# Performance work log

Measured on AMD Instinct MI355X. Metric: run time of the kernel, lower is better.

The kernel has to match this reference:

```python
import jax, jax.numpy as jnp
import numpy as np

B, S, D = 2, 2048, 2048
H, HD = 16, 128
ROPE_THETA = 10000.0


def _rope_cos_sin(seq_len, head_dim, dtype=jnp.float32):
    inv_freq = 1.0 / (ROPE_THETA ** (jnp.arange(0, head_dim, 2, dtype=jnp.float32) / head_dim))
    t = jnp.arange(seq_len, dtype=jnp.float32)
    freqs = jnp.outer(t, inv_freq)                     # [S, HD/2]
    emb = jnp.concatenate([freqs, freqs], axis=-1)     # [S, HD]
    return jnp.cos(emb).astype(dtype), jnp.sin(emb).astype(dtype)


def _rotate_half(x):
    x1, x2 = jnp.split(x, 2, axis=-1)
    return jnp.concatenate([-x2, x1], axis=-1)


def _apply_rope(x, cos, sin):
    # x: [B, S, H, HD]; cos/sin: [S, HD] -> broadcast over batch and heads
    c = cos[None, :, None, :]
    s = sin[None, :, None, :]
    return x * c + _rotate_half(x) * s


def setup_inputs() -> dict:
    key = jax.random.key(0)
    ks = jax.random.split(key, 6)
    scale = 1.0 / np.sqrt(D)
    hidden_states = jax.random.normal(ks[0], (B, S, D), dtype=jnp.float32)
    # causal additive mask: 0 on/below diagonal, large negative above
    neg = jnp.finfo(jnp.float32).min
    causal = jnp.where(jnp.tril(jnp.ones((S, S), dtype=bool)), 0.0, neg)
    attention_mask = jnp.broadcast_to(causal[None, None, :, :], (B, 1, S, S)).astype(jnp.float32)
    Wq = jax.random.normal(ks[1], (D, D), dtype=jnp.float32) * scale
    Wk = jax.random.normal(ks[2], (D, D), dtype=jnp.float32) * scale
    Wv = jax.random.normal(ks[3], (D, D), dtype=jnp.float32) * scale
    Wo = jax.random.normal(ks[4], (D, D), dtype=jnp.float32) * scale
    return {"hidden_states": hidden_states, "attention_mask": attention_mask,
            "Wq": Wq, "Wk": Wk, "Wv": Wv, "Wo": Wo}


def reference(hidden_states, attention_mask, Wq, Wk, Wv, Wo):
    b, s, d = hidden_states.shape
    # projections (torch Linear: x @ W^T)
    q = (hidden_states @ Wq.T).reshape(b, s, H, HD)
    k = (hidden_states @ Wk.T).reshape(b, s, H, HD)
    v = (hidden_states @ Wv.T).reshape(b, s, H, HD)
    cos, sin = _rope_cos_sin(s, HD, hidden_states.dtype)
    q = _apply_rope(q, cos, sin)
    k = _apply_rope(k, cos, sin)
    # naive attention, [B, H, S, S] scores materialized as in the original
    scores = jnp.einsum('bqhd,bkhd->bhqk', q, k) / np.sqrt(HD)
    scores = scores + attention_mask
    attn = jax.nn.softmax(scores, axis=-1)
    out = jnp.einsum('bhqk,bkhd->bqhd', attn, v).reshape(b, s, d)
    return out @ Wo.T
```

## Files before the change

kernel.cpp:

```cpp
#include <hip/hip_runtime.h>
#include <hip/hip_bf16.h>

typedef __hip_bfloat16 bf16;
typedef __attribute__((ext_vector_type(8))) short s16x8;
typedef __attribute__((ext_vector_type(4))) float f32x4;
typedef __attribute__((ext_vector_type(16))) float f32x16;

#define MFMA16(a, b, c) __builtin_amdgcn_mfma_f32_16x16x32_bf16(a, b, c, 0, 0, 0)
#define MFMA32(a, b, c) __builtin_amdgcn_mfma_f32_32x32x16_bf16(a, b, c, 0, 0, 0)

#define GLL16(gsrc, ldst)                                                                 \
  __builtin_amdgcn_global_load_lds(                                                       \
      (const __attribute__((address_space(1))) unsigned int*)(gsrc),                      \
      (__attribute__((address_space(3))) unsigned int*)(ldst), 16, 0, 0)

#define VMCNT(n) asm volatile("s_waitcnt vmcnt(" #n ")" ::: "memory")
#define BARRIER() __builtin_amdgcn_s_barrier()

static constexpr int S_LEN = 2048;
static constexpr int D_DIM = 2048;
static constexpr int NY = 6144;

union BF4 { ushort4 u; bf16 b[4]; };

__device__ inline unsigned pack2(float a, float b) {
  union { bf16 h[2]; unsigned u; } x;
  x.h[0] = __float2bfloat16(a);
  x.h[1] = __float2bfloat16(b);
  return x.u;
}

__global__ void convert_all(const float* __restrict__ X, const float* __restrict__ Wq,
                            const float* __restrict__ Wk, const float* __restrict__ Wv,
                            const float* __restrict__ Wo, bf16* __restrict__ Xb,
                            bf16* __restrict__ Wb, bf16* __restrict__ Wob,
                            float* __restrict__ cosT, float* __restrict__ sinT) {
  int gid = blockIdx.x * 256 + threadIdx.x;
  if (gid < 6291456) {
    int i4 = gid * 4;
    const float* src;
    bf16* dst;
    int off;
    if (i4 < 8388608) {
      src = X; dst = Xb; off = i4;
    } else {
      int j = i4 - 8388608;
      int seg = j >> 22;
      off = j & 4194303;
      if (seg == 0) { src = Wq; dst = Wb; }
      else if (seg == 1) { src = Wk; dst = Wb + 4194304; }
      else if (seg == 2) { src = Wv; dst = Wb + 8388608; }
      else { src = Wo; dst = Wob; }
    }
    float4 v = *(const float4*)(src + off);
    BF4 o;
    o.b[0] = __float2bfloat16(v.x);
    o.b[1] = __float2bfloat16(v.y);
    o.b[2] = __float2bfloat16(v.z);
    o.b[3] = __float2bfloat16(v.w);
    *(ushort4*)(dst + off) = o.u;
  } else {
    int t4 = (gid - 6291456) * 4;
    if (t4 < 131072) {
#pragma unroll
      for (int k = 0; k < 4; ++k) {
        int i = t4 + k;
        int d = i & 63, s = i >> 6;
        float inv = powf(10000.0f, -(float)d * (1.0f / 64.0f));
        float ang = (float)s * inv;
        cosT[i] = cosf(ang);
        sinT[i] = sinf(ang);
      }
    }
  }
}

__global__ __launch_bounds__(256) void rope_tv(bf16* __restrict__ Y,
                                               const float* __restrict__ cosT,
                                               const float* __restrict__ sinT,
                                               bf16* __restrict__ Vt) {
  __shared__ bf16 tile[32][36];
  const int bid = blockIdx.x;
  const int t = threadIdx.x;
  if (bid < 8192) {
    int idx = bid * 256 + t;
    int quad = idx & 15;
    int h = (idx >> 4) & 15;
    int m = (idx >> 8) & 4095;
    int g = idx >> 20;
    int s = m & (S_LEN - 1);
    int d0 = quad * 4;
    float sc = g ? 1.0f : 0.08838834764831845f * 1.4426950408889634f;
    bf16* p = Y + (size_t)m * NY + g * D_DIM + h * 128 + d0;
    BF4 lo, hi, olo, ohi;
    lo.u = *(const ushort4*)p;
    hi.u = *(const ushort4*)(p + 64);
    float4 c = *(const float4*)(cosT + s * 64 + d0);
    float4 sn = *(const float4*)(sinT + s * 64 + d0);
    float cc[4] = {c.x, c.y, c.z, c.w};
    float ss[4] = {sn.x, sn.y, sn.z, sn.w};
#pragma unroll
    for (int i = 0; i < 4; ++i) {
      float x1 = __bfloat162float(lo.b[i]);
      float x2 = __bfloat162float(hi.b[i]);
      olo.b[i] = __float2bfloat16((x1 * cc[i] - x2 * ss[i]) * sc);
      ohi.b[i] = __float2bfloat16((x2 * cc[i] + x1 * ss[i]) * sc);
    }
    *(ushort4*)p = olo.u;
    *(ushort4*)(p + 64) = ohi.u;
  } else {
    int id = bid - 8192;
    int bx = id & 63, by = (id >> 6) & 3, bh = id >> 8;
    int b = bh >> 4, h = bh & 15;
    int s0 = bx * 32, d0 = by * 32;
    int r = t >> 3;
    int c4 = (t & 7) * 4;
    BF4 in;
    in.u = *(const ushort4*)(Y + (size_t)(b * S_LEN + s0 + r) * NY + 4096 + h * 128 + d0 + c4);
    *(ushort4*)(&tile[r][c4]) = in.u;
    __syncthreads();
    BF4 o;
#pragma unroll
    for (int i = 0; i < 4; ++i) o.b[i] = tile[c4 + i][r];
    *(ushort4*)(Vt + (size_t)bh * 128 * S_LEN + (size_t)(d0 + r) * S_LEN + s0 + c4) = o.u;
  }
}

__device__ inline void storeC(float* p, float v) { *p = v; }
__device__ inline void storeC(bf16* p, float v) { *p = __float2bfloat16(v); }

__global__ __launch_bounds__(512, 2) void gemm256(const bf16* __restrict__ A,
                                                  const bf16* __restrict__ Bm,
                                                  bf16* __restrict__ C, int K, int lda,
                                                  int ldb, int ldc, int mt) {
  __shared__ __align__(16) char lds[131072];
  char* A0buf = lds;
  char* B0buf = lds + 32768;
  char* A1buf = lds + 65536;
  char* B1buf = lds + 98304;
  const int tid = threadIdx.x;
  const int lane = tid & 63;
  const int w = tid >> 6;
  const int wm = w >> 2, wn = w & 3;
  const int l15 = lane & 15, lh4 = lane >> 4;
  const int xr = l15 & 7;
  const int xo0 = ((lh4 ^ xr) << 4);
  const int xo1 = (((4 + lh4) ^ xr) << 4);

  const int nwg = gridDim.x;
  const int bid = blockIdx.x;
  const int swz = (bid & 7) * (nwg >> 3) + (bid >> 3);
  const int bm = swz % mt, bn = swz / mt;
  const int row0 = bm * 256, col0 = bn * 256;

  const int srow8 = lane >> 3;
  const int scol = ((lane & 7) ^ srow8) * 8;
  const bf16* gA_s = A + (size_t)(row0 + w * 8 + srow8) * lda + scol;
  const bf16* gB_s = Bm + (size_t)(col0 + (w >> 2) * 64 + (w & 3) * 8 + srow8) * ldb + scol;
  const int ldst = w * 1024;

#define STAGE_A(bufa, rh, k0)                                                     \
  {                                                                               \
    GLL16(gA_s + (size_t)((rh)*64) * lda + (k0), (bufa) + (rh)*16384 + ldst);     \
    GLL16(gA_s + (size_t)((rh)*64 + 128) * lda + (k0),                            \
          (bufa) + (rh)*16384 + 8192 + ldst);                                     \
  }
#define STAGE_B(bufb, ch, k0)                                                     \
  {                                                                               \
    GLL16(gB_s + (size_t)((ch)*32) * ldb + (k0), (bufb) + (ch)*16384 + ldst);     \
    GLL16(gB_s + (size_t)((ch)*32 + 128) * ldb + (k0),                            \
          (bufb) + (ch)*16384 + 8192 + ldst);                                     \
  }

  f32x4 acc[8][4];
#pragma unroll
  for (int i = 0; i < 8; ++i)
#pragma unroll
    for (int j = 0; j < 4; ++j) acc[i][j] = (f32x4){0.f, 0.f, 0.f, 0.f};

  s16x8 af[4][2];
  s16x8 bfr[2][2];

#define READ_AH(bufa, rh)                                                         \
  _Pragma("unroll") for (int ii = 0; ii < 4; ++ii) {                              \
    const char* p_ = (bufa) + (rh)*16384 + (wm * 64 + ii * 16 + l15) * 128;       \
    af[ii][0] = *(const s16x8*)(p_ + xo0);                                        \
    af[ii][1] = *(const s16x8*)(p_ + xo1);                                        \
  }
#define READ_BH(bufb, ch)                                                         \
  _Pragma("unroll") for (int jj = 0; jj < 2; ++jj) {                              \
    const char* p_ = (bufb) + (ch)*16384 + (wn * 32 + jj * 16 + l15) * 128;       \
    bfr[jj][0] = *(const s16x8*)(p_ + xo0);                                       \
    bfr[jj][1] = *(const s16x8*)(p_ + xo1);                                       \
  }
#define QUAD(rh, ch)                                                              \
  __builtin_amdgcn_s_setprio(1);                                                  \
  _Pragma("unroll") for (int jj = 0; jj < 2; ++jj)                                \
  _Pragma("unroll") for (int ii = 0; ii < 4; ++ii)                                \
  _Pragma("unroll") for (int ks = 0; ks < 2; ++ks)                                \
      acc[(rh)*4 + ii][(ch)*2 + jj] =                                             \
          MFMA16(af[ii][ks], bfr[jj][ks], acc[(rh)*4 + ii][(ch)*2 + jj]);         \
  __builtin_amdgcn_s_setprio(0);

  STAGE_A(A0buf, 0, 0);
  STAGE_B(B0buf, 0, 0);
  STAGE_B(B0buf, 1, 0);
  STAGE_A(A0buf, 1, 0);
  STAGE_A(A1buf, 0, 64);
  STAGE_B(B1buf, 1, 64);
  STAGE_A(A1buf, 1, 64);
  VMCNT(6);
  BARRIER();

  const int NI = K >> 7;
  for (int i = 0; i < NI; ++i) {
    const int kT1 = (2 * i + 1) << 6;
    const int kT2 = (2 * i + 2) << 6;
    const int kT3 = (2 * i + 3) << 6;
    const bool nl = (i + 1 < NI);
    READ_AH(A0buf, 0);
    READ_BH(B0buf, 0);
    STAGE_B(B1buf, 0, kT1);
    BARRIER();
    QUAD(0, 0);
    BARRIER();
    READ_BH(B0buf, 1);
    if (nl) STAGE_A(A0buf, 0, kT2);
    BARRIER();
    QUAD(0, 1);
    BARRIER();
    READ_AH(A0buf, 1);
    if (nl) STAGE_B(B0buf, 1, kT2);
    BARRIER();
    QUAD(1, 1);
    BARRIER();
    READ_BH(B0buf, 0);
    if (nl) STAGE_A(A0buf, 1, kT2);
    BARRIER();
    QUAD(1, 0);
    if (nl) { VMCNT(6); } else { VMCNT(0); }
    BARRIER();
    READ_AH(A1buf, 0);
    READ_BH(B1buf, 0);
    if (nl) STAGE_B(B0buf, 0, kT2);
    BARRIER();
    QUAD(0, 0);
    BARRIER();
    READ_BH(B1buf, 1);
    if (nl) STAGE_A(A1buf, 0, kT3);
    BARRIER();
    QUAD(0, 1);
    BARRIER();
    READ_AH(A1buf, 1);
    if (nl) STAGE_B(B1buf, 1, kT3);
    BARRIER();
    QUAD(1, 1);
    BARRIER();
    READ_BH(B1buf, 0);
    if (nl) STAGE_A(A1buf, 1, kT3);
    BARRIER();
    QUAD(1, 0);
    if (nl) { VMCNT(6); }
    BARRIER();
  }
#undef STAGE_A
#undef STAGE_B
#undef READ_AH
#undef READ_BH
#undef QUAD

#pragma unroll
  for (int ri = 0; ri < 8; ++ri)
#pragma unroll
    for (int cj = 0; cj < 4; ++cj) {
      int gr = row0 + wm * 128 + ri * 16 + lh4 * 4;
      int gc = col0 + wn * 64 + cj * 16 + l15;
#pragma unroll
      for (int rr = 0; rr < 4; ++rr)
        C[(size_t)(gr + rr) * ldc + gc] = __float2bfloat16(acc[ri][cj][rr]);
    }
}

template <typename OutT>
__global__ __launch_bounds__(512, 2) void gemm_fine(const bf16* __restrict__ A,
                                                    const bf16* __restrict__ Bm,
                                                    OutT* __restrict__ C, int K, int lda,
                                                    int ldb, int ldc, int mt) {
  __shared__ __align__(16) char lds[147456];
  char* b0 = lds;
  char* b1 = lds + 49152;
  char* b2 = lds + 98304;
  const int tid = threadIdx.x;
  const int lane = tid & 63;
  const int w = tid >> 6;
  const int wm = w >> 2, wn = w & 3;
  const int l15 = lane & 15, lh4 = lane >> 4;
  const int xr = l15 & 7;
  const int xo0 = ((lh4 ^ xr) << 4);
  const int xo1 = (((4 + lh4) ^ xr) << 4);

  const int nwg = gridDim.x;
  const int bid = blockIdx.x;
  const int swz = (bid & 7) * (nwg >> 3) + (bid >> 3);
  const int bm = swz % mt, bn = swz / mt;
  const int row0 = bm * 128, col0 = bn * 256;

  const int srow = w * 8 + (lane >> 3);
  const int scol = ((lane & 7) ^ (lane >> 3)) * 8;
  const bf16* gA = A + (size_t)(row0 + srow) * lda + scol;
  const bf16* gB = Bm + (size_t)(col0 + srow) * ldb + scol;
  const int ldst = w * 1024;

  f32x4 acc[4][4];
#pragma unroll
  for (int i = 0; i < 4; ++i)
#pragma unroll
    for (int j = 0; j < 4; ++j) acc[i][j] = (f32x4){0.f, 0.f, 0.f, 0.f};

  s16x8 af[4], bfr[4];

#define PH_READ(BUF, XO)                                                          \
  _Pragma("unroll") for (int ii = 0; ii < 4; ++ii)                                \
      af[ii] = *(const s16x8*)((BUF) + (wm * 64 + ii * 16 + l15) * 128 + (XO));   \
  _Pragma("unroll") for (int jj = 0; jj < 4; ++jj)                                \
      bfr[jj] = *(const s16x8*)((BUF) + 16384 + (wn * 64 + jj * 16 + l15) * 128 + (XO));
#define PH_FMA()                                                                  \
  __builtin_amdgcn_s_setprio(1);                                                  \
  _Pragma("unroll") for (int jj = 0; jj < 4; ++jj)                                \
  _Pragma("unroll") for (int ii = 0; ii < 4; ++ii)                                \
      acc[ii][jj] = MFMA16(af[ii], bfr[jj], acc[ii][jj]);                         \
  __builtin_amdgcn_s_setprio(0);
#define STAGE_T(BUF, kS)                                                          \
  GLL16(gA + (kS), (BUF) + ldst);                                                 \
  GLL16(gA + (size_t)64 * lda + (kS), (BUF) + 8192 + ldst);                       \
  GLL16(gB + (kS), (BUF) + 16384 + ldst);                                         \
  GLL16(gB + (size_t)64 * ldb + (kS), (BUF) + 24576 + ldst);                      \
  GLL16(gB + (size_t)128 * ldb + (kS), (BUF) + 32768 + ldst);                     \
  GLL16(gB + (size_t)192 * ldb + (kS), (BUF) + 40960 + ldst);
#define TILE_MAIN(RBUF, SBUF, kS)                                                 \
  PH_READ(RBUF, xo0);                                                             \
  GLL16(gA + (kS), (SBUF) + ldst);                                                \
  GLL16(gA + (size_t)64 * lda + (kS), (SBUF) + 8192 + ldst);                      \
  GLL16(gB + (kS), (SBUF) + 16384 + ldst);                                        \
  BARRIER();                                                                      \
  PH_FMA();                                                                       \
  BARRIER();                                                                      \
  PH_READ(RBUF, xo1);                                                             \
  GLL16(gB + (size_t)64 * ldb + (kS), (SBUF) + 24576 + ldst);                     \
  GLL16(gB + (size_t)128 * ldb + (kS), (SBUF) + 32768 + ldst);                    \
  GLL16(gB + (size_t)192 * ldb + (kS), (SBUF) + 40960 + ldst);                    \
  BARRIER();                                                                      \
  PH_FMA();                                                                       \
  VMCNT(6);                                                                       \
  BARRIER();

  STAGE_T(b0, 0);
  STAGE_T(b1, 64);
  VMCNT(6);
  BARRIER();

  const int NT = K >> 6;
  for (int t = 0; t < NT - 2; t += 3) {
    TILE_MAIN(b0, b2, (size_t)(t + 2) * 64);
    TILE_MAIN(b1, b0, (size_t)(t + 3) * 64);
    TILE_MAIN(b2, b1, (size_t)(t + 4) * 64);
  }
  PH_READ(b0, xo0);
  BARRIER();
  PH_FMA();
  BARRIER();
  PH_READ(b0, xo1);
  BARRIER();
  PH_FMA();
  VMCNT(0);
  BARRIER();
  PH_READ(b1, xo0);
  BARRIER();
  PH_FMA();
  BARRIER();
  PH_READ(b1, xo1);
  BARRIER();
  PH_FMA();
#undef PH_READ
#undef PH_FMA
#undef STAGE_T
#undef TILE_MAIN

#pragma unroll
  for (int mi = 0; mi < 4; ++mi)
#pragma unroll
    for (int ni = 0; ni < 4; ++ni) {
      int gr = row0 + wm * 64 + mi * 16 + lh4 * 4;
      int gc = col0 + wn * 64 + ni * 16 + l15;
#pragma unroll
      for (int rr = 0; rr < 4; ++rr)
        storeC(&C[(size_t)(gr + rr) * ldc + gc], acc[mi][ni][rr]);
    }
}

__global__ __launch_bounds__(256, 2) void attn_fwd(const bf16* __restrict__ Y,
                                                   const bf16* __restrict__ Vt,
                                                   bf16* __restrict__ At) {
  __shared__ __align__(16) char smem[65536];

  const int idx = blockIdx.x;
  const int qt = 15 - (idx >> 5);
  const int bh = idx & 31;
  const int b = bh >> 4, h = bh & 15;
  const int tid = threadIdx.x;
  const int lane = tid & 63;
  const int w = tid >> 6;
  const int l31 = lane & 31;
  const int hi = lane >> 5;
  const int q0w = qt * 128 + w * 32;
  const int q = q0w + l31;

  s16x8 qf[8];
  {
    const bf16* qb = Y + (size_t)(b * S_LEN + q) * NY + h * 128 + hi * 8;
#pragma unroll
    for (int s = 0; s < 8; ++s) qf[s] = *(const s16x8*)(qb + s * 16);
  }

  f32x16 O[4];
#pragma unroll
  for (int d = 0; d < 4; ++d)
#pragma unroll
    for (int e = 0; e < 16; ++e) O[d][e] = 0.f;
  float m_run = -3.0e38f, l_run = 0.f;

  const bf16* Kbase = Y + (size_t)(b * S_LEN) * NY + 2048 + h * 128;
  const bf16* Vbase = Vt + (size_t)bh * 128 * S_LEN;
  const int tmax = 2 * qt + 1;

  const int rk_ = w * 4 + (lane >> 4);
  const int ck_ = lane & 15;
  const int dv_ = w * 8 + (lane >> 3);
  const int cv_ = lane & 7;

#define STAGE_KV(T, BASE)                                                         \
  {                                                                               \
    const int kv0s = (T)*64;                                                      \
    _Pragma("unroll") for (int j = 0; j < 4; ++j) {                               \
      int rk = j * 16 + rk_;                                                      \
      GLL16(Kbase + (size_t)(kv0s + rk) * NY + ((ck_ ^ (rk & 15)) * 8),           \
            (BASE) + (j * 4096 + w * 1024));                                      \
      int dv = j * 32 + dv_;                                                      \
      GLL16(Vbase + (size_t)dv * S_LEN + kv0s + ((cv_ ^ (dv & 7)) * 8),           \
            (BASE) + 16384 + (j * 4096 + w * 1024));                              \
    }                                                                             \
  }

  STAGE_KV(0, smem);

  for (int t = 0; t <= tmax; ++t) {
    const int kv0 = t * 64;
    const char* cur = smem + (t & 1) * 32768;
    BARRIER();
    if (t < tmax) {
      STAGE_KV(t + 1, smem + ((t + 1) & 1) * 32768);
      VMCNT(8);
    } else {
      VMCNT(0);
    }
    BARRIER();
    if (kv0 > q0w + 31) continue;

    float sv[32];
#pragma unroll
    for (int tt = 0; tt < 2; ++tt) {
      f32x16 sa;
#pragma unroll
      for (int e = 0; e < 16; ++e) sa[e] = 0.f;
      const int rk = tt * 32 + l31;
      const char* kr = cur + rk * 256;
      const int xr = (rk & 15) << 4;
#pragma unroll
      for (int s = 0; s < 8; ++s) {
        s16x8 kf = *(const s16x8*)(kr + ((s * 32 + hi * 16) ^ xr));
        sa = MFMA32(kf, qf[s], sa);
      }
#pragma unroll
      for (int e = 0; e < 16; ++e) sv[tt * 16 + e] = sa[e];
    }

    if (kv0 + 63 > q0w) {
#pragma unroll
      for (int tt = 0; tt < 2; ++tt)
#pragma unroll
        for (int r = 0; r < 16; ++r) {
          int kvr = kv0 + tt * 32 + (r & 3) + 8 * (r >> 2) + 4 * hi;
          if (kvr > q) sv[tt * 16 + r] = -3.0e38f;
        }
    }

    float mx[16];
#pragma unroll
    for (int i = 0; i < 16; ++i) mx[i] = fmaxf(sv[i], sv[i + 16]);
#pragma unroll
    for (int st = 8; st >= 1; st >>= 1)
#pragma unroll
      for (int i = 0; i < 8; ++i)
        if (i < st) mx[i] = fmaxf(mx[i], mx[i + st]);
    float pmax = fmaxf(mx[0], __shfl_xor(mx[0], 32, 64));

    bool need = pmax > m_run + 11.54f;
    if (__any(need)) {
      float newm = fmaxf(m_run, pmax);
      float ef = exp2f(m_run - newm);
      m_run = newm;
      l_run *= ef;
#pragma unroll
      for (int d = 0; d < 4; ++d)
#pragma unroll
        for (int e = 0; e < 16; ++e) O[d][e] *= ef;
    }

    float rsum = 0.f;
#pragma unroll
    for (int i = 0; i < 32; ++i) {
      sv[i] = exp2f(sv[i] - m_run);
      rsum += sv[i];
    }
    rsum += __shfl_xor(rsum, 32, 64);
    l_run += rsum;

    unsigned pw[4][4];
#pragma unroll
    for (int tt = 0; tt < 2; ++tt) {
      const int bs = tt * 16;
      unsigned x01 = pack2(sv[bs + 0], sv[bs + 1]);
      unsigned x23 = pack2(sv[bs + 2], sv[bs + 3]);
      unsigned x45 = pack2(sv[bs + 4], sv[bs + 5]);
      unsigned x67 = pack2(sv[bs + 6], sv[bs + 7]);
      unsigned y01 = pack2(sv[bs + 8], sv[bs + 9]);
      unsigned y23 = pack2(sv[bs + 10], sv[bs + 11]);
      unsigned y45 = pack2(sv[bs + 12], sv[bs + 13]);
      unsigned y67 = pack2(sv[bs + 14], sv[bs + 15]);
      asm volatile("v_permlane32_swap_b32 %0, %1" : "+v"(x01), "+v"(x45));
      asm volatile("v_permlane32_swap_b32 %0, %1" : "+v"(x23), "+v"(x67));
      asm volatile("v_permlane32_swap_b32 %0, %1" : "+v"(y01), "+v"(y45));
      asm volatile("v_permlane32_swap_b32 %0, %1" : "+v"(y23), "+v"(y67));
      pw[tt * 2][0] = x01;
      pw[tt * 2][1] = x23;
      pw[tt * 2][2] = x45;
      pw[tt * 2][3] = x67;
      pw[tt * 2 + 1][0] = y01;
      pw[tt * 2 + 1][1] = y23;
      pw[tt * 2 + 1][2] = y45;
      pw[tt * 2 + 1][3] = y67;
    }

#pragma unroll
    for (int dt = 0; dt < 4; ++dt) {
      const int d = dt * 32 + l31;
      const char* vr = cur + 16384 + d * 128;
      const int xv = (d & 7) << 4;
#pragma unroll
      for (int sl = 0; sl < 4; ++sl) {
        s16x8 vf = *(const s16x8*)(vr + ((sl * 32 + hi * 16) ^ xv));
        union { unsigned u[4]; s16x8 v; } pb;
        pb.u[0] = pw[sl][0];
        pb.u[1] = pw[sl][1];
        pb.u[2] = pw[sl][2];
        pb.u[3] = pw[sl][3];
        O[dt] = MFMA32(vf, pb.v, O[dt]);
      }
    }
  }
#undef STAGE_KV

  __syncthreads();
  const float inv = 1.0f / l_run;
  {
    const int orow = w * 32 + l31;
    const int xo = (orow & 15) << 4;
    char* obase = (char*)smem + orow * 256;
#pragma unroll
    for (int dt = 0; dt < 4; ++dt)
#pragma unroll
      for (int r = 0; r < 16; ++r) {
        int d = dt * 32 + (r & 3) + 8 * (r >> 2) + 4 * hi;
        *(bf16*)(obase + ((d * 2) ^ xo)) = __float2bfloat16(O[dt][r] * inv);
      }
  }
  __syncthreads();
  bf16* dst = At + (size_t)(b * S_LEN + qt * 128) * D_DIM + h * 128;
#pragma unroll
  for (int j = 0; j < 8; ++j) {
    int id = j * 256 + tid;
    int rr = id >> 4, cc = id & 15;
    int4 val = *(const int4*)((char*)smem + rr * 256 + ((cc * 16) ^ ((rr & 15) << 4)));
    *(int4*)(dst + (size_t)rr * D_DIM + cc * 8) = val;
  }
}

extern "C" void kernel_launch(void* const* d_in, const int* in_sizes, int n_in,
                              void* d_out, int out_size, void* d_ws, size_t ws_size,
                              hipStream_t stream) {
  const float* X = (const float*)d_in[0];
  const float* Wq = (const float*)d_in[2];
  const float* Wk = (const float*)d_in[3];
  const float* Wv = (const float*)d_in[4];
  const float* Wo = (const float*)d_in[5];
  float* out = (float*)d_out;
  char* ws = (char*)d_ws;

  bf16* Xb = (bf16*)(ws);
  bf16* Wb = (bf16*)(ws + 16777216);
  bf16* Wob = (bf16*)(ws + 41943040);
  bf16* Y = (bf16*)(ws + 50331648);
  bf16* Vt = (bf16*)(ws + 100663296);
  bf16* At = (bf16*)(ws + 117440512);
  float* cosT = (float*)(ws + 134217728);
  float* sinT = (float*)(ws + 134742016);

  convert_all<<<24704, 256, 0, stream>>>(X, Wq, Wk, Wv, Wo, Xb, Wb, Wob, cosT, sinT);

  gemm256<<<256, 512, 0, stream>>>(Xb, Wb, Y, 2048, 2048, 2048, 6144, 16);
  gemm_fine<bf16><<<256, 512, 0, stream>>>(Xb, Wb + (size_t)4096 * 2048, Y + 4096,
                                           2048, 2048, 2048, 6144, 32);
  rope_tv<<<16384, 256, 0, stream>>>(Y, cosT, sinT, Vt);
  attn_fwd<<<512, 256, 0, stream>>>(Y, Vt, At);
  gemm_fine<float><<<256, 512, 0, stream>>>(At, Wob, out, 2048, 2048, 2048, 2048, 32);
}
```

Baseline: 247.8 us.

## Software-pipeline attention: overlap next QK^T with current softmax and PV

Restructures the causal flash-attention loop so the QK^T MFMA for tile t+1 is issued before the softmax and PV of tile t, with K double-buffered and V triple-buffered in a larger LDS allocation. It also adds s_setprio around MFMA blocks, splits QK accumulation into two independent chains, and uses tree reductions for max and sum. The launch index mapping now handles blocks beyond 256. The goal is to hide MFMA and exp latency behind each other, at the cost of more registers and LDS (80KB), which may lower occupancy relative to the requested 2 blocks per CU.

```diff
diff --git a/kernel.cpp b/kernel.cpp
--- a/kernel.cpp
+++ b/kernel.cpp
@@ -401,10 +401,10 @@
 __global__ __launch_bounds__(256, 2) void attn_fwd(const bf16* __restrict__ Y,
                                                    const bf16* __restrict__ Vt,
                                                    bf16* __restrict__ At) {
-  __shared__ __align__(16) char smem[65536];
+  __shared__ __align__(16) char smem[81920];
 
   const int idx = blockIdx.x;
-  const int qt = 15 - (idx >> 5);
+  const int qt = (idx < 256) ? (15 - (idx >> 5)) : ((idx - 256) >> 5);
   const int bh = idx & 31;
   const int b = bh >> 4, h = bh & 15;
   const int tid = threadIdx.x;
@@ -412,6 +412,7 @@
   const int w = tid >> 6;
   const int l31 = lane & 31;
   const int hi = lane >> 5;
+  const int hi4 = hi * 4;
   const int q0w = qt * 128 + w * 32;
   const int q = q0w + l31;
 
@@ -437,138 +438,166 @@
   const int ck_ = lane & 15;
   const int dv_ = w * 8 + (lane >> 3);
   const int cv_ = lane & 7;
-
-#define STAGE_KV(T, BASE)                                                         \
+  char* const Vlds = smem + 32768;
+
+#define STAGE_KV(T, KOFF, VOFF)                                                   \
   {                                                                               \
     const int kv0s = (T)*64;                                                      \
     _Pragma("unroll") for (int j = 0; j < 4; ++j) {                               \
       int rk = j * 16 + rk_;                                                      \
       GLL16(Kbase + (size_t)(kv0s + rk) * NY + ((ck_ ^ (rk & 15)) * 8),           \
-            (BASE) + (j * 4096 + w * 1024));                                      \
+            smem + (KOFF) + (j * 4096 + w * 1024));                               \
       int dv = j * 32 + dv_;                                                      \
       GLL16(Vbase + (size_t)dv * S_LEN + kv0s + ((cv_ ^ (dv & 7)) * 8),           \
-            (BASE) + 16384 + (j * 4096 + w * 1024));                              \
+            Vlds + (VOFF) + (j * 4096 + w * 1024));                               \
     }                                                                             \
   }
 
-  STAGE_KV(0, smem);
-
-  for (int t = 0; t <= tmax; ++t) {
-    const int kv0 = t * 64;
-    const char* cur = smem + (t & 1) * 32768;
-    BARRIER();
-    if (t < tmax) {
-      STAGE_KV(t + 1, smem + ((t + 1) & 1) * 32768);
-      VMCNT(8);
-    } else {
-      VMCNT(0);
-    }
-    BARRIER();
-    if (kv0 > q0w + 31) continue;
-
-    float sv[32];
-#pragma unroll
-    for (int tt = 0; tt < 2; ++tt) {
-      f32x16 sa;
-#pragma unroll
-      for (int e = 0; e < 16; ++e) sa[e] = 0.f;
-      const int rk = tt * 32 + l31;
-      const char* kr = cur + rk * 256;
-      const int xr = (rk & 15) << 4;
-#pragma unroll
-      for (int s = 0; s < 8; ++s) {
-        s16x8 kf = *(const s16x8*)(kr + ((s * 32 + hi * 16) ^ xr));
-        sa = MFMA32(kf, qf[s], sa);
-      }
-#pragma unroll
-      for (int e = 0; e < 16; ++e) sv[tt * 16 + e] = sa[e];
-    }
-
-    if (kv0 + 63 > q0w) {
-#pragma unroll
-      for (int tt = 0; tt < 2; ++tt)
-#pragma unroll
-        for (int r = 0; r < 16; ++r) {
-          int kvr = kv0 + tt * 32 + (r & 3) + 8 * (r >> 2) + 4 * hi;
-          if (kvr > q) sv[tt * 16 + r] = -3.0e38f;
-        }
-    }
-
-    float mx[16];
-#pragma unroll
-    for (int i = 0; i < 16; ++i) mx[i] = fmaxf(sv[i], sv[i + 16]);
-#pragma unroll
-    for (int st = 8; st >= 1; st >>= 1)
-#pragma unroll
-      for (int i = 0; i < 8; ++i)
-        if (i < st) mx[i] = fmaxf(mx[i], mx[i + st]);
-    float pmax = fmaxf(mx[0], __shfl_xor(mx[0], 32, 64));
-
-    bool need = pmax > m_run + 11.54f;
-    if (__any(need)) {
-      float newm = fmaxf(m_run, pmax);
-      float ef = exp2f(m_run - newm);
-      m_run = newm;
-      l_run *= ef;
-#pragma unroll
-      for (int d = 0; d < 4; ++d)
-#pragma unroll
-        for (int e = 0; e < 16; ++e) O[d][e] *= ef;
-    }
-
-    float rsum = 0.f;
-#pragma unroll
-    for (int i = 0; i < 32; ++i) {
-      sv[i] = exp2f(sv[i] - m_run);
-      rsum += sv[i];
-    }
-    rsum += __shfl_xor(rsum, 32, 64);
-    l_run += rsum;
-
-    unsigned pw[4][4];
-#pragma unroll
-    for (int tt = 0; tt < 2; ++tt) {
-      const int bs = tt * 16;
-      unsigned x01 = pack2(sv[bs + 0], sv[bs + 1]);
-      unsigned x23 = pack2(sv[bs + 2], sv[bs + 3]);
-      unsigned x45 = pack2(sv[bs + 4], sv[bs + 5]);
-      unsigned x67 = pack2(sv[bs + 6], sv[bs + 7]);
-      unsigned y01 = pack2(sv[bs + 8], sv[bs + 9]);
-      unsigned y23 = pack2(sv[bs + 10], sv[bs + 11]);
-      unsigned y45 = pack2(sv[bs + 12], sv[bs + 13]);
-      unsigned y67 = pack2(sv[bs + 14], sv[bs + 15]);
-      asm volatile("v_permlane32_swap_b32 %0, %1" : "+v"(x01), "+v"(x45));
-      asm volatile("v_permlane32_swap_b32 %0, %1" : "+v"(x23), "+v"(x67));
-      asm volatile("v_permlane32_swap_b32 %0, %1" : "+v"(y01), "+v"(y45));
-      asm volatile("v_permlane32_swap_b32 %0, %1" : "+v"(y23), "+v"(y67));
-      pw[tt * 2][0] = x01;
-      pw[tt * 2][1] = x23;
-      pw[tt * 2][2] = x45;
-      pw[tt * 2][3] = x67;
-      pw[tt * 2 + 1][0] = y01;
-      pw[tt * 2 + 1][1] = y23;
-      pw[tt * 2 + 1][2] = y45;
-      pw[tt * 2 + 1][3] = y67;
-    }
-
-#pragma unroll
-    for (int dt = 0; dt < 4; ++dt) {
-      const int d = dt * 32 + l31;
-      const char* vr = cur + 16384 + d * 128;
-      const int xv = (d & 7) << 4;
-#pragma unroll
-      for (int sl = 0; sl < 4; ++sl) {
-        s16x8 vf = *(const s16x8*)(vr + ((sl * 32 + hi * 16) ^ xv));
-        union { unsigned u[4]; s16x8 v; } pb;
-        pb.u[0] = pw[sl][0];
-        pb.u[1] = pw[sl][1];
-        pb.u[2] = pw[sl][2];
-        pb.u[3] = pw[sl][3];
-        O[dt] = MFMA32(vf, pb.v, O[dt]);
-      }
-    }
-  }
+#define QKT(SVC, KOFF)                                                            \
+  {                                                                               \
+    __builtin_amdgcn_s_setprio(1);                                                \
+    _Pragma("unroll") for (int tt = 0; tt < 2; ++tt) {                            \
+      f32x16 se, so;                                                              \
+      _Pragma("unroll") for (int e = 0; e < 16; ++e) { se[e] = 0.f; so[e] = 0.f; }\
+      const int rk = tt * 32 + l31;                                               \
+      const char* kr = smem + (KOFF) + rk * 256;                                  \
+      const int xrr = (rk & 15) << 4;                                             \
+      _Pragma("unroll") for (int s = 0; s < 8; s += 2) {                          \
+        s16x8 kf0 = *(const s16x8*)(kr + ((s * 32 + hi * 16) ^ xrr));             \
+        se = MFMA32(kf0, qf[s], se);                                              \
+        s16x8 kf1 = *(const s16x8*)(kr + (((s + 1) * 32 + hi * 16) ^ xrr));       \
+        so = MFMA32(kf1, qf[s + 1], so);                                          \
+      }                                                                           \
+      _Pragma("unroll") for (int e = 0; e < 16; ++e) SVC[tt * 16 + e] = se[e] + so[e]; \
+    }                                                                             \
+    __builtin_amdgcn_s_setprio(0);                                                \
+  }
+
+#define FIN_A(SVP, KV0P)                                                          \
+  {                                                                               \
+    if ((KV0P) + 63 > q0w) {                                                      \
+      const int thr = q - (KV0P);                                                 \
+      _Pragma("unroll") for (int tt = 0; tt < 2; ++tt)                            \
+      _Pragma("unroll") for (int r = 0; r < 16; ++r) {                            \
+        const int c = tt * 32 + (r & 3) + 8 * (r >> 2);                           \
+        SVP[tt * 16 + r] = (c + hi4 > thr) ? -3.0e38f : SVP[tt * 16 + r];         \
+      }                                                                           \
+    }                                                                             \
+    float m8[8];                                                                  \
+    _Pragma("unroll") for (int i = 0; i < 8; ++i)                                 \
+        m8[i] = fmaxf(fmaxf(SVP[i], SVP[i + 8]), fmaxf(SVP[i + 16], SVP[i + 24]));\
+    float m2a = fmaxf(fmaxf(m8[0], m8[1]), fmaxf(m8[2], m8[3]));                  \
+    float m2b = fmaxf(fmaxf(m8[4], m8[5]), fmaxf(m8[6], m8[7]));                  \
+    float mloc = fmaxf(m2a, m2b);                                                 \
+    float pmax = fmaxf(mloc, __shfl_xor(mloc, 32, 64));                           \
+    bool need = pmax > m_run + 11.54f;                                            \
+    if (__any(need)) {                                                            \
+      float newm = fmaxf(m_run, pmax);                                            \
+      float ef = exp2f(m_run - newm);                                             \
+      m_run = newm;                                                               \
+      l_run *= ef;                                                                \
+      _Pragma("unroll") for (int d = 0; d < 4; ++d)                               \
+      _Pragma("unroll") for (int e = 0; e < 16; ++e) O[d][e] *= ef;               \
+    }                                                                             \
+  }
+
+#define FIN_B(SVP, VOFF)                                                          \
+  {                                                                               \
+    _Pragma("unroll") for (int i = 0; i < 32; ++i) SVP[i] = exp2f(SVP[i] - m_run);\
+    float s16v[16];                                                               \
+    _Pragma("unroll") for (int i = 0; i < 16; ++i) s16v[i] = SVP[i] + SVP[i + 16];\
+    float s8v[8];                                                                 \
+    _Pragma("unroll") for (int i = 0; i < 8; ++i) s8v[i] = s16v[i] + s16v[i + 8]; \
+    float s4v[4];                                                                 \
+    _Pragma("unroll") for (int i = 0; i < 4; ++i) s4v[i] = s8v[i] + s8v[i + 4];   \
+    float rsum = (s4v[0] + s4v[1]) + (s4v[2] + s4v[3]);                           \
+    rsum += __shfl_xor(rsum, 32, 64);                                             \
+    l_run += rsum;                                                                \
+    unsigned pw[4][4];                                                            \
+    _Pragma("unroll") for (int tt = 0; tt < 2; ++tt) {                            \
+      const int bs = tt * 16;                                                     \
+      unsigned x01 = pack2(SVP[bs + 0], SVP[bs + 1]);                             \
+      unsigned x23 = pack2(SVP[bs + 2], SVP[bs + 3]);                             \
+      unsigned x45 = pack2(SVP[bs + 4], SVP[bs + 5]);                             \
+      unsigned x67 = pack2(SVP[bs + 6], SVP[bs + 7]);                             \
+      unsigned y01 = pack2(SVP[bs + 8], SVP[bs + 9]);                             \
+      unsigned y23 = pack2(SVP[bs + 10], SVP[bs + 11]);                           \
+      unsigned y45 = pack2(SVP[bs + 12], SVP[bs + 13]);                           \
+      unsigned y67 = pack2(SVP[bs + 14], SVP[bs + 15]);                           \
+      asm volatile("v_permlane32_swap_b32 %0, %1" : "+v"(x01), "+v"(x45));        \
+      asm volatile("v_permlane32_swap_b32 %0, %1" : "+v"(x23), "+v"(x67));        \
+      asm volatile("v_permlane32_swap_b32 %0, %1" : "+v"(y01), "+v"(y45));        \
+      asm volatile("v_permlane32_swap_b32 %0, %1" : "+v"(y23), "+v"(y67));        \
+      pw[tt * 2][0] = x01; pw[tt * 2][1] = x23;                                   \
+      pw[tt * 2][2] = x45; pw[tt * 2][3] = x67;                                   \
+      pw[tt * 2 + 1][0] = y01; pw[tt * 2 + 1][1] = y23;                           \
+      pw[tt * 2 + 1][2] = y45; pw[tt * 2 + 1][3] = y67;                           \
+    }                                                                             \
+    __builtin_amdgcn_s_setprio(1);                                                \
+    _Pragma("unroll") for (int dt = 0; dt < 4; ++dt) {                            \
+      const int d = dt * 32 + l31;                                                \
+      const char* vr = Vlds + (VOFF) + d * 128;                                   \
+      const int xv = (d & 7) << 4;                                                \
+      _Pragma("unroll") for (int sl = 0; sl < 4; ++sl) {                          \
+        s16x8 vf = *(const s16x8*)(vr + ((sl * 32 + hi * 16) ^ xv));              \
+        union { unsigned u[4]; s16x8 v; } pb;                                     \
+        pb.u[0] = pw[sl][0]; pb.u[1] = pw[sl][1];                                 \
+        pb.u[2] = pw[sl][2]; pb.u[3] = pw[sl][3];                                 \
+        O[dt] = MFMA32(vf, pb.v, O[dt]);                                          \
+      }                                                                           \
+    }                                                                             \
+    __builtin_amdgcn_s_setprio(0);                                                \
+  }
+
+#define ROT3(x) ((x) = ((x) == 32768 ? 0 : (x) + 16384))
+
+  float sv0[32], sv1[32];
+
+  STAGE_KV(0, 0, 0);
+  BARRIER();
+  STAGE_KV(1, 16384, 16384);
+  VMCNT(8);
+  BARRIER();
+  QKT(sv0, 0);
+
+  int vstg = 32768;
+  int vprv = 0;
+
+  for (int t = 1; t < tmax; t += 2) {
+    BARRIER();
+    STAGE_KV(t + 1, 0, vstg);
+    ROT3(vstg);
+    VMCNT(8);
+    BARRIER();
+    QKT(sv1, 16384);
+    FIN_A(sv0, (t - 1) * 64);
+    FIN_B(sv0, vprv);
+    ROT3(vprv);
+    BARRIER();
+    STAGE_KV(t + 2, 16384, vstg);
+    ROT3(vstg);
+    VMCNT(8);
+    BARRIER();
+    QKT(sv0, 0);
+    FIN_A(sv1, t * 64);
+    FIN_B(sv1, vprv);
+    ROT3(vprv);
+  }
+  BARRIER();
+  VMCNT(0);
+  BARRIER();
+  QKT(sv1, 16384);
+  FIN_A(sv0, (tmax - 1) * 64);
+  FIN_B(sv0, vprv);
+  ROT3(vprv);
+  FIN_A(sv1, tmax * 64);
+  FIN_B(sv1, vprv);
+
 #undef STAGE_KV
+#undef QKT
+#undef FIN_A
+#undef FIN_B
+#undef ROT3
 
   __syncthreads();
   const float inv = 1.0f / l_run;
```

After: 291.9 us. 1.18x slower.
